# Kernel optimization log

Measured on AMD Instinct MI355X. Metric: run time of the kernel, lower is better.

## Reference

```python
import jax, jax.numpy as jnp
import numpy as np

B, T, V, H = 4, 512, 8000, 7


def setup_inputs() -> dict:
    key = jax.random.key(0)
    k1, k2, k3 = jax.random.split(key, 3)
    return {
        "input_ids": jax.random.randint(k1, (B, T), 0, V),
        "frequencies": jax.random.normal(k2, (V,), dtype=jnp.float32) * 3.0,
        "amplitudes": 1.0 + jax.random.normal(k3, (V,), dtype=jnp.float32) * 0.1,
        "decay": jnp.asarray(1.5, dtype=jnp.float32),
        "chunk_size": 16,
    }


def reference(input_ids, frequencies, amplitudes, decay, chunk_size):
    h = jnp.arange(1, H + 1, dtype=frequencies.dtype)  # (H,)
    # harmonic expansion: freqs = f*[1..H], amps = A/[1..H]^decay
    all_f = frequencies[:, None] * h                    # (V, H)
    all_A = amplitudes[:, None] / h ** decay            # (V, H)
    seq_f = frequencies[input_ids][..., None] * h       # (B, T, H)
    seq_A = amplitudes[input_ids][..., None] / h ** decay

    nc = T // chunk_size
    sfc = seq_f.reshape(B, nc, chunk_size, H).transpose(1, 0, 2, 3)  # (nc,B,c,H)
    sAc = seq_A.reshape(B, nc, chunk_size, H).transpose(1, 0, 2, 3)

    def per_chunk(args):
        sf, sA = args  # (B,c,H)
        df = sf[:, :, :, None, None] - all_f[None, None, None, :, :]   # (B,c,H,V,H)
        amp = sA[:, :, :, None, None] * all_A[None, None, None, :, :]
        return 2.0 * (amp * jnp.sinc(2.0 * df)).sum(axis=(2, 4))       # (B,c,V)

    Cc = jax.lax.map(per_chunk, (sfc, sAc))            # (nc, B, c, V)
    C = Cc.transpose(1, 0, 2, 3).reshape(B, T, V)      # (B, T, V)

    cum = jnp.cumsum(C, axis=1)
    # logits[t] uses history 0..t-1 -> shift right by one, position 0 gets zeros
    logits = jnp.concatenate([jnp.zeros_like(cum[:, :1]), cum[:, :-1]], axis=1)
    return logits
```

## Files before the change

### kernel.cpp

```cpp
#include <hip/hip_runtime.h>
#include <math.h>


typedef float v2f __attribute__((ext_vector_type(2)));
typedef float v4f __attribute__((ext_vector_type(4)));

constexpr int cB = 4, cT = 512, cV = 8000, cH = 7;
constexpr int GT = 16;
constexpr int NSEG = cT / GT;
constexpr int NPLANE = 28;

__device__ __forceinline__ v2f pk_add(v2f a, v2f b) {
    v2f d; asm("v_pk_add_f32 %0, %1, %2" : "=v"(d) : "v"(a), "v"(b)); return d;
}
__device__ __forceinline__ v2f pk_mul(v2f a, v2f b) {
    v2f d; asm("v_pk_mul_f32 %0, %1, %2" : "=v"(d) : "v"(a), "v"(b)); return d;
}
__device__ __forceinline__ v2f pk_fma(v2f a, v2f b, v2f c) {
    v2f d; asm("v_pk_fma_f32 %0, %1, %2, %3" : "=v"(d) : "v"(a), "v"(b), "v"(c));
    return d;
}

__global__ __launch_bounds__(256) void wavelm_tab(
    const float* __restrict__ freq, const float* __restrict__ amp,
    const float* __restrict__ decay_p, float* __restrict__ tab)
{
    const int v = blockIdx.x * 256 + threadIdx.x;
    if (v >= cV) return;
    const float decay = decay_p[0];
    const float f = freq[v], A = amp[v];
    const float p2 = __builtin_amdgcn_exp2f(-decay);
    const float p3 = __builtin_amdgcn_exp2f(-decay * 1.5849625007f);
    const float p5 = __builtin_amdgcn_exp2f(-decay * 2.3219280949f);
    const float p7 = __builtin_amdgcn_exp2f(-decay * 2.8073549221f);
    const float rp[7] = {1.f, p2, p3, p2*p2, p5, p2*p3, p7};
    const float xr = f - rintf(f);
    const float s1 = __builtin_amdgcn_sinf(xr);
    const float c1 = __builtin_amdgcn_cosf(xr);
    float s = s1, c = c1;
#pragma unroll
    for (int k = 0; k < cH; ++k) {
        if (k) { const float sp = s, cp = c;
                 s = fmaf(sp, c1,  cp * s1);
                 c = fmaf(cp, c1, -(sp * s1)); }
        tab[(size_t)k * cV + v]        = s;
        tab[(size_t)(7 + k) * cV + v]  = c;
        tab[(size_t)(14 + k) * cV + v] = A * rp[k];
        tab[(size_t)(21 + k) * cV + v] = f * (float)(k + 1);
    }
}

__global__ __launch_bounds__(256) void wavelm_g(
    const int* __restrict__ ids, const float* __restrict__ tab,
    float* __restrict__ out, float* __restrict__ segsum, const int segmode)
{
    const int bs  = blockIdx.y;
    const int bt0 = bs * GT;
    const int vh  = blockIdx.x * 256 + threadIdx.x;
    const bool valid = (vh * 2 < cV);
    const int vc = valid ? vh : 0;

    const v2f* tp = (const v2f*)tab;
    v2f nb[cH], sBw[cH], cBw[cH];
#pragma unroll
    for (int j = 0; j < cH; ++j) {
        const v2f s = tp[(size_t)j * (cV/2) + vc];
        const v2f c = tp[(size_t)(7 + j) * (cV/2) + vc];
        const v2f w = tp[(size_t)(14 + j) * (cV/2) + vc];
        const v2f a = tp[(size_t)(21 + j) * (cV/2) + vc];
        const v2f ws = w * 0.15915494309189535f;
        sBw[j] = s * ws;
        cBw[j] = c * ws;
        nb[j].x = -a.x;  nb[j].y = -a.y;
    }

    v2f acc;  acc.x = 0.f;  acc.y = 0.f;

    int idc = ids[bt0];
    for (int g = 0; g < GT; ++g) {
        const int idn = (g + 1 < GT) ? ids[bt0 + g + 1] : idc;

        float sA[cH], cA[cH], wA[cH], aU[cH];
#pragma unroll
        for (int i = 0; i < cH; ++i) {
            sA[i] = tab[(size_t)i * cV + idc];
            cA[i] = tab[(size_t)(7 + i) * cV + idc];
            wA[i] = tab[(size_t)(14 + i) * cV + idc];
            aU[i] = tab[(size_t)(21 + i) * cV + idc];
        }

        float accx = 0.f, accy = 0.f;
        float mn = 3.0e38f, mx = 0.0f;
#pragma unroll
        for (int i = 0; i < cH; ++i) {
            v2f ai;  ai.x = aU[i];  ai.y = aU[i];
            v2f d[cH], p[cH];
#pragma unroll
            for (int j = 0; j < cH; ++j) d[j] = pk_add(ai, nb[j]);
            p[0] = d[0];
#pragma unroll
            for (int j = 1; j < cH; ++j) p[j] = pk_mul(p[j-1], d[j]);
            const float ptot = p[6].x * p[6].y;
            mn = fminf(mn, fminf(fabsf(p[6].x), fabsf(p[6].y)));
            mn = fminf(mn, fabsf(ptot));
            mx = fmaxf(mx, fabsf(ptot));
            const float rt = __builtin_amdgcn_rcpf(ptot);
            v2f r;  r.x = rt * p[6].y;  r.y = rt * p[6].x;
            v2f accS = (v2f)0.f, accC = (v2f)0.f;
#pragma unroll
            for (int j = cH - 1; j >= 1; --j) {
                const v2f inv = pk_mul(r, p[j-1]);
                accS = pk_fma(cBw[j], inv, accS);
                accC = pk_fma(sBw[j], inv, accC);
                r = pk_mul(r, d[j]);
            }
            accS = pk_fma(cBw[0], r, accS);
            accC = pk_fma(sBw[0], r, accC);
            const float tx = fmaf(sA[i], accS.x, -(cA[i] * accC.x));
            const float ty = fmaf(sA[i], accS.y, -(cA[i] * accC.y));
            accx = fmaf(wA[i], tx, accx);
            accy = fmaf(wA[i], ty, accy);
        }

        if (mn < 1e-37f || mx > 1e37f) {
            accx = 0.f;  accy = 0.f;
#pragma unroll
            for (int i = 0; i < cH; ++i) {
                float ax = 0.f, ay = 0.f;
#pragma unroll
                for (int j = 0; j < cH; ++j) {
                    const v2f w = tp[(size_t)(14 + j) * (cV/2) + vc];
                    const float dx = aU[i] + nb[j].x;
                    const float dy = aU[i] + nb[j].y;
                    const float snx = fmaf(sA[i], cBw[j].x, -(cA[i] * sBw[j].x));
                    const float sny = fmaf(sA[i], cBw[j].y, -(cA[i] * sBw[j].y));
                    float qx = snx * __builtin_amdgcn_rcpf(dx);
                    float qy = sny * __builtin_amdgcn_rcpf(dy);
                    qx = (dx == 0.f) ? w.x : qx;
                    qy = (dy == 0.f) ? w.y : qy;
                    ax += qx;  ay += qy;
                }
                accx = fmaf(wA[i], ax, accx);
                accy = fmaf(wA[i], ay, accy);
            }
        }

        if (valid) {
            v2f res;  res.x = 2.f * accx;  res.y = 2.f * accy;
            const size_t o = (size_t)(bt0 + g) * cV + (size_t)vh * 2;
            v2f wv;  wv.x = segmode ? acc.x : res.x;
                     wv.y = segmode ? acc.y : res.y;
            *(v2f*)(out + o) = wv;
            acc = pk_add(acc, res);
        }

        idc = idn;
    }

    if (valid && segmode)
        *(v2f*)(segsum + (size_t)bs * cV + (size_t)vh * 2) = acc;
}

__global__ __launch_bounds__(256) void wavelm_bases(float* __restrict__ segsum)
{
    const int g = blockIdx.x * 256 + threadIdx.x;
    if (g >= cB * cV) return;
    const int b = g / cV;
    const int v = g - b * cV;
    float* p = segsum + (size_t)b * NSEG * cV + v;
    float acc = 0.f;
#pragma unroll
    for (int s = 0; s < NSEG; ++s) {
        const float t = p[(size_t)s * cV];
        p[(size_t)s * cV] = acc;
        acc += t;
    }
}

__global__ __launch_bounds__(256) void wavelm_addbase(
    float* __restrict__ out, const float* __restrict__ bases)
{
    const int btq = blockIdx.y;
    const int b  = btq >> 6;
    const int t0 = (btq & 63) * 8;
    const int seg = t0 / GT;
    if (seg == 0) return;
    const int v4 = blockIdx.x * 256 + threadIdx.x;
    if (v4 >= cV / 4) return;

    const v4f base = *(const v4f*)(bases +
        ((size_t)(b * NSEG + seg)) * cV + (size_t)v4 * 4);
    float* p = out + ((size_t)b * cT + t0) * cV + (size_t)v4 * 4;
#pragma unroll
    for (int k = 0; k < 8; ++k) {
        v4f x = *(v4f*)(p + (size_t)k * cV);
        x.x += base.x;  x.y += base.y;  x.z += base.z;  x.w += base.w;
        *(v4f*)(p + (size_t)k * cV) = x;
    }
}

__global__ __launch_bounds__(256) void wavelm_scan(float* __restrict__ out)
{
    const int g = blockIdx.x * blockDim.x + threadIdx.x;
    if (g >= cB * cV) return;
    const int b = g / cV;
    const int v = g - b * cV;
    float* p = out + (size_t)b * cT * cV + v;
    float acc = 0.f;
#pragma unroll 8
    for (int t = 0; t < cT; ++t) {
        const float c = p[(size_t)t * cV];
        p[(size_t)t * cV] = acc;
        acc += c;
    }
}

extern "C" void kernel_launch(void* const* d_in, const int* in_sizes, int n_in,
                              void* d_out, int out_size, void* d_ws, size_t ws_size,
                              hipStream_t stream)
{
    const int*   ids  = (const int*)d_in[0];
    const float* freq = (const float*)d_in[1];
    const float* amp  = (const float*)d_in[2];
    const float* dec  = (const float*)d_in[3];
    float* out = (float*)d_out;
    float* tab = (float*)d_ws;
    float* segsum = tab + (size_t)NPLANE * cV;

    const size_t tab_b = (size_t)NPLANE * cV * sizeof(float);
    const size_t seg_b = (size_t)cB * NSEG * cV * sizeof(float);
    const int segmode = (tab_b + seg_b <= ws_size) ? 1 : 0;

    wavelm_tab<<<(cV + 255) / 256, 256, 0, stream>>>(freq, amp, dec, tab);

    dim3 grid((cV / 2 + 255) / 256, cB * cT / GT);
    wavelm_g<<<grid, dim3(256), 0, stream>>>(ids, tab, out, segsum, segmode);

    if (segmode) {
        const int nchains = cB * cV;
        wavelm_bases<<<(nchains + 255) / 256, dim3(256), 0, stream>>>(segsum);
        dim3 ab((cV / 4 + 255) / 256, cB * (cT / 8));
        wavelm_addbase<<<ab, dim3(256), 0, stream>>>(out, segsum);
    } else {
        const int nchains = cB * cV;
        wavelm_scan<<<(nchains + 255) / 256, dim3(256), 0, stream>>>(out);
    }
}
```

Measured before the change: 216.4 us.

## Recompute per-token harmonics in registers and fold segment-base scan into addbase

The main kernel now loads only four table values per token (base sin/cos, amplitude, frequency) instead of 28. It regenerates the harmonic sin/cos with angle-addition recurrences, computes the decay weights from the decay scalar via exp2, and factors the amplitude out into the final scale. The separate segment-prefix kernel is removed, and addbase instead sums the preceding segment partials directly, which saves one launch but makes later segments read more data. The recurrence adds ALU work and may shift rounding slightly.

```diff
diff --git a/kernel.cpp b/kernel.cpp
--- a/kernel.cpp
+++ b/kernel.cpp
@@ -52,6 +52,7 @@
 
 __global__ __launch_bounds__(256) void wavelm_g(
     const int* __restrict__ ids, const float* __restrict__ tab,
+    const float* __restrict__ decay_p,
     float* __restrict__ out, float* __restrict__ segsum, const int segmode)
 {
     const int bs  = blockIdx.y;
@@ -74,26 +75,34 @@
         nb[j].x = -a.x;  nb[j].y = -a.y;
     }
 
+    const float decay = decay_p[0];
+    const float q2 = __builtin_amdgcn_exp2f(-decay);
+    const float q3 = __builtin_amdgcn_exp2f(-decay * 1.5849625007f);
+    const float q5 = __builtin_amdgcn_exp2f(-decay * 2.3219280949f);
+    const float q7 = __builtin_amdgcn_exp2f(-decay * 2.8073549221f);
+    const float rp[7] = {1.f, q2, q3, q2*q2, q5, q2*q3, q7};
+
     v2f acc;  acc.x = 0.f;  acc.y = 0.f;
 
     int idc = ids[bt0];
     for (int g = 0; g < GT; ++g) {
         const int idn = (g + 1 < GT) ? ids[bt0 + g + 1] : idc;
 
-        float sA[cH], cA[cH], wA[cH], aU[cH];
-#pragma unroll
-        for (int i = 0; i < cH; ++i) {
-            sA[i] = tab[(size_t)i * cV + idc];
-            cA[i] = tab[(size_t)(7 + i) * cV + idc];
-            wA[i] = tab[(size_t)(14 + i) * cV + idc];
-            aU[i] = tab[(size_t)(21 + i) * cV + idc];
-        }
+        const float fu  = tab[(size_t)21 * cV + idc];
+        const float Au  = tab[(size_t)14 * cV + idc];
+        const float s1u = tab[idc];
+        const float c1u = tab[(size_t)7 * cV + idc];
 
         float accx = 0.f, accy = 0.f;
         float mn = 3.0e38f, mx = 0.0f;
+        float su = s1u, cu = c1u;
 #pragma unroll
         for (int i = 0; i < cH; ++i) {
-            v2f ai;  ai.x = aU[i];  ai.y = aU[i];
+            if (i) { const float sp = su, cp = cu;
+                     su = fmaf(sp, c1u,  cp * s1u);
+                     cu = fmaf(cp, c1u, -(sp * s1u)); }
+            const float au = fu * (float)(i + 1);
+            v2f ai;  ai.x = au;  ai.y = au;
             v2f d[cH], p[cH];
 #pragma unroll
             for (int j = 0; j < cH; ++j) d[j] = pk_add(ai, nb[j]);
@@ -116,37 +125,43 @@
             }
             accS = pk_fma(cBw[0], r, accS);
             accC = pk_fma(sBw[0], r, accC);
-            const float tx = fmaf(sA[i], accS.x, -(cA[i] * accC.x));
-            const float ty = fmaf(sA[i], accS.y, -(cA[i] * accC.y));
-            accx = fmaf(wA[i], tx, accx);
-            accy = fmaf(wA[i], ty, accy);
+            const float tx = fmaf(su, accS.x, -(cu * accC.x));
+            const float ty = fmaf(su, accS.y, -(cu * accC.y));
+            accx = fmaf(rp[i], tx, accx);
+            accy = fmaf(rp[i], ty, accy);
         }
 
         if (mn < 1e-37f || mx > 1e37f) {
             accx = 0.f;  accy = 0.f;
+            float s2 = s1u, c2 = c1u;
 #pragma unroll
             for (int i = 0; i < cH; ++i) {
+                if (i) { const float sp = s2, cp = c2;
+                         s2 = fmaf(sp, c1u,  cp * s1u);
+                         c2 = fmaf(cp, c1u, -(sp * s1u)); }
+                const float au = fu * (float)(i + 1);
                 float ax = 0.f, ay = 0.f;
 #pragma unroll
                 for (int j = 0; j < cH; ++j) {
                     const v2f w = tp[(size_t)(14 + j) * (cV/2) + vc];
-                    const float dx = aU[i] + nb[j].x;
-                    const float dy = aU[i] + nb[j].y;
-                    const float snx = fmaf(sA[i], cBw[j].x, -(cA[i] * sBw[j].x));
-                    const float sny = fmaf(sA[i], cBw[j].y, -(cA[i] * sBw[j].y));
+                    const float dx = au + nb[j].x;
+                    const float dy = au + nb[j].y;
+                    const float snx = fmaf(s2, cBw[j].x, -(c2 * sBw[j].x));
+                    const float sny = fmaf(s2, cBw[j].y, -(c2 * sBw[j].y));
                     float qx = snx * __builtin_amdgcn_rcpf(dx);
                     float qy = sny * __builtin_amdgcn_rcpf(dy);
                     qx = (dx == 0.f) ? w.x : qx;
                     qy = (dy == 0.f) ? w.y : qy;
                     ax += qx;  ay += qy;
                 }
-                accx = fmaf(wA[i], ax, accx);
-                accy = fmaf(wA[i], ay, accy);
+                accx = fmaf(rp[i], ax, accx);
+                accy = fmaf(rp[i], ay, accy);
             }
         }
 
         if (valid) {
-            v2f res;  res.x = 2.f * accx;  res.y = 2.f * accy;
+            const float A2 = 2.f * Au;
+            v2f res;  res.x = A2 * accx;  res.y = A2 * accy;
             const size_t o = (size_t)(bt0 + g) * cV + (size_t)vh * 2;
             v2f wv;  wv.x = segmode ? acc.x : res.x;
                      wv.y = segmode ? acc.y : res.y;
@@ -161,24 +176,8 @@
         *(v2f*)(segsum + (size_t)bs * cV + (size_t)vh * 2) = acc;
 }
 
-__global__ __launch_bounds__(256) void wavelm_bases(float* __restrict__ segsum)
-{
-    const int g = blockIdx.x * 256 + threadIdx.x;
-    if (g >= cB * cV) return;
-    const int b = g / cV;
-    const int v = g - b * cV;
-    float* p = segsum + (size_t)b * NSEG * cV + v;
-    float acc = 0.f;
-#pragma unroll
-    for (int s = 0; s < NSEG; ++s) {
-        const float t = p[(size_t)s * cV];
-        p[(size_t)s * cV] = acc;
-        acc += t;
-    }
-}
-
 __global__ __launch_bounds__(256) void wavelm_addbase(
-    float* __restrict__ out, const float* __restrict__ bases)
+    float* __restrict__ out, const float* __restrict__ segsum)
 {
     const int btq = blockIdx.y;
     const int b  = btq >> 6;
@@ -188,8 +187,13 @@
     const int v4 = blockIdx.x * 256 + threadIdx.x;
     if (v4 >= cV / 4) return;
 
-    const v4f base = *(const v4f*)(bases +
-        ((size_t)(b * NSEG + seg)) * cV + (size_t)v4 * 4);
+    const float* sp = segsum + (size_t)b * NSEG * cV + (size_t)v4 * 4;
+    v4f base;  base.x = 0.f;  base.y = 0.f;  base.z = 0.f;  base.w = 0.f;
+    for (int s = 0; s < seg; ++s) {
+        const v4f x = *(const v4f*)(sp + (size_t)s * cV);
+        base.x += x.x;  base.y += x.y;  base.z += x.z;  base.w += x.w;
+    }
+
     float* p = out + ((size_t)b * cT + t0) * cV + (size_t)v4 * 4;
 #pragma unroll
     for (int k = 0; k < 8; ++k) {
@@ -234,11 +238,9 @@
     wavelm_tab<<<(cV + 255) / 256, 256, 0, stream>>>(freq, amp, dec, tab);
 
     dim3 grid((cV / 2 + 255) / 256, cB * cT / GT);
-    wavelm_g<<<grid, dim3(256), 0, stream>>>(ids, tab, out, segsum, segmode);
+    wavelm_g<<<grid, dim3(256), 0, stream>>>(ids, tab, dec, out, segsum, segmode);
 
     if (segmode) {
-        const int nchains = cB * cV;
-        wavelm_bases<<<(nchains + 255) / 256, dim3(256), 0, stream>>>(segsum);
         dim3 ab((cV / 4 + 255) / 256, cB * (cT / 8));
         wavelm_addbase<<<ab, dim3(256), 0, stream>>>(out, segsum);
     } else {
```

After: 212.0 us. 1.02x faster.
